# Kernel tuning notes

Hardware: AMD Instinct MI355X
Metric: run time of the kernel (lower is better)

## Reference

```python
import jax, jax.numpy as jnp
import numpy as np

EMBED = 2048
NUM_HEADS = 32
HEAD_DIM = EMBED // NUM_HEADS  # 64 (original head dim; sets the scaling)
RANK_KQ = 1024
RANK_V = 1024
DK = RANK_KQ // NUM_HEADS  # 32 low-rank kq head dim
DV = RANK_V // NUM_HEADS   # 32 low-rank v head dim
B, S = 2, 2048


def setup_inputs() -> dict:
    key = jax.random.key(0)
    ks = jax.random.split(key, 10)
    std = 0.02
    hidden_states = jax.random.normal(ks[0], (B, S, EMBED), dtype=jnp.float32)
    # causal additive mask, shape (B, 1, S, S) as asserted in forward
    neg = jnp.finfo(jnp.float32).min
    causal = jnp.where(jnp.tril(jnp.ones((S, S), dtype=bool)), 0.0, neg)
    attention_mask = jnp.broadcast_to(causal[None, None], (B, 1, S, S)).astype(jnp.float32)
    Wq = jax.random.normal(ks[1], (RANK_KQ, EMBED), dtype=jnp.float32) * std
    bq = jax.random.normal(ks[2], (RANK_KQ,), dtype=jnp.float32) * std
    Wk = jax.random.normal(ks[3], (RANK_KQ, EMBED), dtype=jnp.float32) * std
    bk = jax.random.normal(ks[4], (RANK_KQ,), dtype=jnp.float32) * std
    Wv = jax.random.normal(ks[5], (RANK_V, EMBED), dtype=jnp.float32) * std
    bv = jax.random.normal(ks[6], (RANK_V,), dtype=jnp.float32) * std
    Wo = jax.random.normal(ks[7], (EMBED, RANK_V), dtype=jnp.float32) * std
    bo = jax.random.normal(ks[8], (EMBED,), dtype=jnp.float32) * std
    return {"hidden_states": hidden_states, "attention_mask": attention_mask,
            "Wq": Wq, "bq": bq, "Wk": Wk, "bk": bk, "Wv": Wv, "bv": bv,
            "Wo": Wo, "bo": bo}


def reference(hidden_states, attention_mask, Wq, bq, Wk, bk, Wv, bv, Wo, bo):
    bsz, tgt_len, _ = hidden_states.shape
    scaling = HEAD_DIM ** (-0.5)  # uses ORIGINAL head_dim, not low-rank dim

    def split_heads(x, d):  # (b, s, H*d) -> (b, H, s, d)
        return x.reshape(bsz, -1, NUM_HEADS, d).transpose(0, 2, 1, 3)

    q = split_heads((hidden_states @ Wq.T + bq) * scaling, DK)
    k = split_heads(hidden_states @ Wk.T + bk, DK)
    v = split_heads(hidden_states @ Wv.T + bv, DV)

    # scores: (b, H, tgt, src)
    attn = jnp.einsum('bhqd,bhkd->bhqk', q, k)
    attn = attn + attention_mask  # broadcast over heads
    attn = jnp.maximum(attn, jnp.finfo(attn.dtype).min)
    attn = jax.nn.softmax(attn, axis=-1)

    out = jnp.einsum('bhqk,bhkd->bhqd', attn, v)  # (b, H, tgt, DV)
    out = out.transpose(0, 2, 1, 3).reshape(bsz, tgt_len, RANK_V)
    return out @ Wo.T + bo
```

## Files before the change

### kernel.cpp

```cpp
#include <hip/hip_runtime.h>
#include <stdint.h>

typedef __attribute__((ext_vector_type(8))) short bf16x8;
typedef __attribute__((ext_vector_type(4))) float f32x4;
typedef unsigned short ushort_t;

#define AS1 __attribute__((address_space(1)))
#define AS3 __attribute__((address_space(3)))

static __device__ __forceinline__ ushort_t f2b(float f) {
    union { float f; unsigned u; } x; x.f = f;
    unsigned r = x.u + 0x7fffu + ((x.u >> 16) & 1u);
    return (ushort_t)(r >> 16);
}
static __device__ __forceinline__ f32x4 mfma16(bf16x8 a, bf16x8 b, f32x4 c) {
    return __builtin_amdgcn_mfma_f32_16x16x32_bf16(a, b, c, 0, 0, 0);
}
static __device__ __forceinline__ void gl_lds16(const ushort_t* g, ushort_t* l) {
    __builtin_amdgcn_global_load_lds((const AS1 void*)g, (AS3 void*)l, 16, 0, 0);
}
static __device__ __forceinline__ unsigned pk2(float a, float b) {
    unsigned r;
    asm("v_cvt_pk_bf16_f32 %0, %1, %2" : "=v"(r) : "v"(a), "v"(b));
    return r;
}

__global__ __launch_bounds__(256)
void cvt_bf16(const float* __restrict__ s, ushort_t* __restrict__ d, int n8)
{
    int i = blockIdx.x * 256 + threadIdx.x;
    if (i >= n8) return;
    const float* p = s + (size_t)i * 8;
    f32x4 a = *(const f32x4*)p;
    f32x4 b = *(const f32x4*)(p + 4);
    bf16x8 r;
#pragma unroll
    for (int j = 0; j < 4; ++j) { r[j] = (short)f2b(a[j]); r[j+4] = (short)f2b(b[j]); }
    *(bf16x8*)(d + (size_t)i * 8) = r;
}

__global__ __launch_bounds__(256)
void cvt_w3(const float* __restrict__ wq, const float* __restrict__ wk,
            const float* __restrict__ wv, ushort_t* __restrict__ d)
{
    const float* s = (blockIdx.y == 0) ? wq : (blockIdx.y == 1) ? wk : wv;
    ushort_t* dst = d + (size_t)blockIdx.y * 2097152;
    int i = blockIdx.x * 256 + threadIdx.x;
    const float* p = s + (size_t)i * 8;
    f32x4 a = *(const f32x4*)p;
    f32x4 b = *(const f32x4*)(p + 4);
    bf16x8 r;
#pragma unroll
    for (int j = 0; j < 4; ++j) { r[j] = (short)f2b(a[j]); r[j+4] = (short)f2b(b[j]); }
    *(bf16x8*)(dst + (size_t)i * 8) = r;
}

__global__ __launch_bounds__(256, 2)
void gemm_nt(const ushort_t* __restrict__ A, const ushort_t* __restrict__ B,
             const float* __restrict__ b0, const float* __restrict__ b1,
             const float* __restrict__ b2, void* __restrict__ Cv,
             int M, int N, int K, float scale, int epi)
{
    __shared__ __align__(16) ushort_t As[128 * 32];
    __shared__ __align__(16) ushort_t Bs[128 * 32];
    const int tid = threadIdx.x;
    const int wave = tid >> 6, lane = tid & 63;
    const int l16 = lane & 15, quad = lane >> 4;
    const int bm = blockIdx.x * 128, bn = blockIdx.y * 128;
    const int wm = (wave >> 1) * 64, wn = (wave & 1) * 64;

    f32x4 acc[4][4];
#pragma unroll
    for (int i = 0; i < 4; ++i)
#pragma unroll
        for (int j = 0; j < 4; ++j) acc[i][j] = (f32x4){0.f, 0.f, 0.f, 0.f};

    for (int k0 = 0; k0 < K; k0 += 32) {
        __syncthreads();
#pragma unroll
        for (int i = 0; i < 2; ++i) {
            int chunk = i * 256 + tid;
            int row = chunk >> 2, c8 = chunk & 3;
            gl_lds16(A + (size_t)(bm + row) * K + k0 + c8 * 8, As + chunk * 8);
            gl_lds16(B + (size_t)(bn + row) * K + k0 + c8 * 8, Bs + chunk * 8);
        }
        __syncthreads();
        bf16x8 af[4], bfr[4];
#pragma unroll
        for (int i = 0; i < 4; ++i)
            af[i] = *(const bf16x8*)(As + (wm + i * 16 + l16) * 32 + quad * 8);
#pragma unroll
        for (int j = 0; j < 4; ++j)
            bfr[j] = *(const bf16x8*)(Bs + (wn + j * 16 + l16) * 32 + quad * 8);
#pragma unroll
        for (int i = 0; i < 4; ++i)
#pragma unroll
            for (int j = 0; j < 4; ++j)
                acc[i][j] = mfma16(af[i], bfr[j], acc[i][j]);
    }

#pragma unroll
    for (int i = 0; i < 4; ++i) {
#pragma unroll
        for (int j = 0; j < 4; ++j) {
            int col = bn + wn + j * 16 + l16;
            if (epi == 0) {
                float bvs = b0[col];
#pragma unroll
                for (int r = 0; r < 4; ++r) {
                    int row = bm + wm + i * 16 + quad * 4 + r;
                    ((float*)Cv)[(size_t)row * N + col] = (acc[i][j][r] + bvs) * scale;
                }
            } else {
                int mat = col >> 10, nc = col & 1023;
                const float* bp = (mat == 0) ? b0 : (mat == 1) ? b1 : b2;
                float bvs = bp[nc];
                int h = nc >> 5, d = nc & 31;
                if (mat == 2) {
                    int row0 = bm + wm + i * 16 + quad * 4;
                    int b = row0 >> 11, s = row0 & 2047;
                    ushort_t* dst = (ushort_t*)Cv + (size_t)2 * 4194304
                                  + ((size_t)(b * 32 + h) * 32 + d) * 2048 + s;
                    uint2 w;
                    w.x = ((unsigned)f2b(acc[i][j][1] + bvs) << 16) | f2b(acc[i][j][0] + bvs);
                    w.y = ((unsigned)f2b(acc[i][j][3] + bvs) << 16) | f2b(acc[i][j][2] + bvs);
                    *(uint2*)dst = w;
                } else {
                    float sc = (mat == 0) ? 0.125f : 1.0f;
                    ushort_t* dst = (ushort_t*)Cv + (size_t)mat * 4194304;
#pragma unroll
                    for (int r = 0; r < 4; ++r) {
                        int row = bm + wm + i * 16 + quad * 4 + r;
                        int b = row >> 11, s = row & 2047;
                        float v = (acc[i][j][r] + bvs) * sc;
                        dst[(((size_t)(b * 32 + h) * 2048 + s) << 5) + d] = f2b(v);
                    }
                }
            }
        }
    }
}

__global__ __launch_bounds__(512, 1)
void gemm8b(const ushort_t* __restrict__ A, const ushort_t* __restrict__ B,
            const float* __restrict__ bias, float* __restrict__ C,
            int M, int N, int K, float scale)
{
    __shared__ __align__(16) ushort_t lds[49152];
    const int tid = threadIdx.x;
    const int wave = tid >> 6, lane = tid & 63;
    const int l16 = lane & 15, quad = lane >> 4;
    const int wr = wave >> 2, wc = wave & 3;
    const int bm = blockIdx.x * 128, bn = blockIdx.y * 256;
    const int xo = (l16 & 8) << 1;
    const int S = K >> 4;
    const int NT = K >> 7;

    f32x4 acc[4][4];
#pragma unroll
    for (int i = 0; i < 4; ++i)
#pragma unroll
        for (int j = 0; j < 4; ++j) acc[i][j] = (f32x4){0.f,0.f,0.f,0.f};

    auto stg = [&](int s_) {
        int r = s_ & 7;
        ushort_t* ldst = lds + (r >> 1) * 12288 + (r & 1) * 8192;
        int ko = (s_ >> 1) << 5;
        if (s_ & 1) {
            int c = tid;
            int cl = c ^ (((c >> 5) & 1) << 1);
            gl_lds16(A + (size_t)(bm + (cl >> 2)) * K + ko + (cl & 3) * 8,
                     ldst + c * 8);
        } else {
#pragma unroll
            for (int call = 0; call < 2; ++call) {
                int c = call * 512 + tid;
                int cl = c ^ (((c >> 5) & 1) << 1);
                gl_lds16(B + (size_t)(bn + (cl >> 2)) * K + ko + (cl & 3) * 8,
                         ldst + c * 8);
            }
        }
    };

#pragma unroll
    for (int s0 = 0; s0 < 7; ++s0) stg(s0);
    asm volatile("s_waitcnt vmcnt(5)" ::: "memory");
    __builtin_amdgcn_s_barrier();

    for (int t = 0; t < NT; ++t) {
        const bool lastit = (t == NT - 1);
        bf16x8 bfr[4], af[2];
#pragma unroll
        for (int p = 0; p < 8; ++p) {
            asm volatile("" ::: "memory");
            const int offB = (p >> 1) * 12288;
            const int offA = offB + 8192;
            if ((p & 1) == 0) {
#pragma unroll
                for (int j = 0; j < 4; ++j)
                    bfr[j] = *(const bf16x8*)(lds + offB
                              + (wc * 64 + j * 16 + l16) * 32 + ((quad * 8) ^ xo));
            }
#pragma unroll
            for (int m = 0; m < 2; ++m)
                af[m] = *(const bf16x8*)(lds + offA
                          + (wr * 64 + (p & 1) * 32 + m * 16 + l16) * 32
                          + ((quad * 8) ^ xo));
            { int s_ = 8 * t + 7 + p; if (s_ < S) stg(s_); }
            __builtin_amdgcn_s_barrier();
            asm volatile("s_waitcnt lgkmcnt(0)" ::: "memory");
            __builtin_amdgcn_sched_barrier(0);
            __builtin_amdgcn_s_setprio(1);
#pragma unroll
            for (int m = 0; m < 2; ++m)
#pragma unroll
                for (int j = 0; j < 4; ++j)
                    acc[(p & 1) * 2 + m][j] =
                        mfma16(af[m], bfr[j], acc[(p & 1) * 2 + m][j]);
            __builtin_amdgcn_s_setprio(0);
            if (p == 3) {
                if (lastit) asm volatile("s_waitcnt vmcnt(0)" ::: "memory");
                else        asm volatile("s_waitcnt vmcnt(5)" ::: "memory");
            } else if (p == 7) {
                if (!lastit) asm volatile("s_waitcnt vmcnt(5)" ::: "memory");
            }
            __builtin_amdgcn_s_barrier();
        }
    }

#pragma unroll
    for (int i = 0; i < 4; ++i) {
#pragma unroll
        for (int j = 0; j < 4; ++j) {
            int col = bn + wc * 64 + j * 16 + l16;
            float bvs = bias[col];
#pragma unroll
            for (int r = 0; r < 4; ++r) {
                int row = bm + wr * 64 + i * 16 + quad * 4 + r;
                C[(size_t)row * N + col] = (acc[i][j][r] + bvs) * scale;
            }
        }
    }
}

__global__ __launch_bounds__(256, 4)
void attn(const ushort_t* __restrict__ Q, const ushort_t* __restrict__ Kg,
          const ushort_t* __restrict__ VT, ushort_t* __restrict__ Ctx)
{
    __shared__ __align__(16) ushort_t Ps[4][32 * 72];
    const int tid = threadIdx.x, wave = tid >> 6, lane = tid & 63;
    const int l16 = lane & 15, quad = lane >> 4, quad4 = quad * 4;
    const int bh = blockIdx.x;
    const int pr = blockIdx.y;
    const ushort_t* Qh = Q  + (size_t)bh * 2048 * 32;
    const ushort_t* Kh = Kg + (size_t)bh * 2048 * 32;
    const ushort_t* Vh = VT + (size_t)bh * 32 * 2048;
    const int b = bh >> 5, h = bh & 31;
    ushort_t* P0 = &Ps[wave][0];

    for (int half = 0; half < 2; ++half) {
        const int qt = half ? (15 - pr) : pr;
        const int q0 = qt * 128 + wave * 32;

        bf16x8 qf0 = *(const bf16x8*)(Qh + (size_t)(q0 + l16) * 32 + quad * 8);
        bf16x8 qf1 = *(const bf16x8*)(Qh + (size_t)(q0 + 16 + l16) * 32 + quad * 8);

        f32x4 o00 = (f32x4){0.f,0.f,0.f,0.f}, o01 = o00, o10 = o00, o11 = o00;
        float rs0 = 0.f, rs1 = 0.f;

        const int nchw = ((q0 + 31) >> 6) + 1;
        for (int c = 0; c < nchw; ++c) {
            const int kv0 = c * 64;
            bf16x8 kf[4];
#pragma unroll
            for (int t = 0; t < 4; ++t)
                kf[t] = *(const bf16x8*)(Kh + (size_t)(kv0 + t * 16 + l16) * 32 + quad * 8);
            f32x4 st0[4], st1[4];
#pragma unroll
            for (int t = 0; t < 4; ++t) {
                st0[t] = mfma16(kf[t], qf0, (f32x4){0.f,0.f,0.f,0.f});
                st1[t] = mfma16(kf[t], qf1, (f32x4){0.f,0.f,0.f,0.f});
            }
            bf16x8 vA0 = *(const bf16x8*)(Vh + (size_t)l16 * 2048 + kv0 + quad * 8);
            bf16x8 vA1 = *(const bf16x8*)(Vh + (size_t)l16 * 2048 + kv0 + 32 + quad * 8);
            bf16x8 vB0 = *(const bf16x8*)(Vh + (size_t)(16 + l16) * 2048 + kv0 + quad * 8);
            bf16x8 vB1 = *(const bf16x8*)(Vh + (size_t)(16 + l16) * 2048 + kv0 + 32 + quad * 8);

            const int qk0 = q0 + l16 - kv0;
            auto softmax_pack = [&](bool masked) {
#pragma unroll
                for (int t = 0; t < 4; ++t) {
                    float p0[4], p1[4];
#pragma unroll
                    for (int r = 0; r < 4; ++r) {
                        const int kk = t * 16 + quad4 + r;
                        float e0 = __expf(st0[t][r]);
                        float e1 = __expf(st1[t][r]);
                        p0[r] = (!masked || kk <= qk0)      ? e0 : 0.f;
                        p1[r] = (!masked || kk <= qk0 + 16) ? e1 : 0.f;
                        rs0 += p0[r]; rs1 += p1[r];
                    }
                    uint2 w0, w1;
                    w0.x = pk2(p0[0], p0[1]); w0.y = pk2(p0[2], p0[3]);
                    w1.x = pk2(p1[0], p1[1]); w1.y = pk2(p1[2], p1[3]);
                    *(uint2*)(P0 + (size_t)l16 * 72 + t * 16 + quad4) = w0;
                    *(uint2*)(P0 + (size_t)(16 + l16) * 72 + t * 16 + quad4) = w1;
                }
            };
            if (kv0 + 63 <= q0) softmax_pack(false); else softmax_pack(true);

            asm volatile("s_waitcnt lgkmcnt(0)" ::: "memory");
#pragma unroll
            for (int ks = 0; ks < 2; ++ks) {
                bf16x8 pa0 = *(const bf16x8*)(P0 + (size_t)l16 * 72 + ks * 32 + quad * 8);
                bf16x8 pa1 = *(const bf16x8*)(P0 + (size_t)(16 + l16) * 72 + ks * 32 + quad * 8);
                bf16x8 va = ks ? vA1 : vA0;
                bf16x8 vb = ks ? vB1 : vB0;
                o00 = mfma16(pa0, va, o00);
                o01 = mfma16(pa0, vb, o01);
                o10 = mfma16(pa1, va, o10);
                o11 = mfma16(pa1, vb, o11);
            }
        }

        rs0 += __shfl_xor(rs0, 16); rs0 += __shfl_xor(rs0, 32);
        rs1 += __shfl_xor(rs1, 16); rs1 += __shfl_xor(rs1, 32);

#pragma unroll
        for (int r = 0; r < 4; ++r) {
            const int qr = q0 + quad4 + r;
            float inv0 = 1.0f / __shfl(rs0, quad4 + r);
            float inv1 = 1.0f / __shfl(rs1, quad4 + r);
            size_t base0 = ((size_t)b * 2048 + qr) * 1024 + h * 32;
            size_t base1 = ((size_t)b * 2048 + qr + 16) * 1024 + h * 32;
            Ctx[base0 + l16]      = f2b(o00[r] * inv0);
            Ctx[base0 + 16 + l16] = f2b(o01[r] * inv0);
            Ctx[base1 + l16]      = f2b(o10[r] * inv1);
            Ctx[base1 + 16 + l16] = f2b(o11[r] * inv1);
        }
    }
}

extern "C" void kernel_launch(void* const* d_in, const int* in_sizes, int n_in,
                              void* d_out, int out_size, void* d_ws, size_t ws_size,
                              hipStream_t stream)
{
    const float* H  = (const float*)d_in[0];
    const float* Wq = (const float*)d_in[2];
    const float* bq = (const float*)d_in[3];
    const float* Wk = (const float*)d_in[4];
    const float* bk = (const float*)d_in[5];
    const float* Wv = (const float*)d_in[6];
    const float* bv = (const float*)d_in[7];
    const float* Wo = (const float*)d_in[8];
    const float* bo = (const float*)d_in[9];

    ushort_t* Hb   = (ushort_t*)d_ws;
    ushort_t* Wcat = Hb   + (size_t)8388608;
    ushort_t* Qb   = Wcat + (size_t)6291456;
    ushort_t* Kb   = Qb   + (size_t)4194304;
    ushort_t* Vtb  = Kb   + (size_t)4194304;
    ushort_t* Ctx  = Vtb  + (size_t)4194304;
    ushort_t* Wob  = Hb;

    dim3 blk(256, 1, 1);
    hipLaunchKernelGGL(cvt_bf16, dim3(4096, 1, 1), blk, 0, stream, H, Hb, 1048576);
    hipLaunchKernelGGL(cvt_w3, dim3(1024, 3, 1), blk, 0, stream, Wq, Wk, Wv, Wcat);

    hipLaunchKernelGGL(gemm_nt, dim3(32, 24, 1), blk, 0, stream,
                       Hb, Wcat, bq, bk, bv, (void*)Qb, 4096, 3072, 2048, 1.0f, 2);

    hipLaunchKernelGGL(cvt_bf16, dim3(1024, 1, 1), blk, 0, stream, Wo, Wob, 262144);

    hipLaunchKernelGGL(attn, dim3(64, 8, 1), blk, 0, stream, Qb, Kb, Vtb, Ctx);

    hipLaunchKernelGGL(gemm8b, dim3(32, 8, 1), dim3(512, 1, 1), 0, stream,
                       Ctx, Wob, bo, (float*)d_out, 4096, 2048, 1024, 1.0f);
}
```

Measured before the change: 279.8 us.

## Triple-buffer QKV GEMM LDS loads with swizzle and single barrier per step

Rewrites the QKV projection GEMM to use a three-slot LDS ring, prefetching tiles two k-steps ahead with global_load_lds and waiting on vmcnt, so only one barrier per iteration is needed. It XOR-swizzles the LDS layout to reduce bank conflicts on fragment reads, raises the MFMA priority during compute, and raises the launch-bounds occupancy hint to 3 blocks. The goal is to hide global-load latency behind the MFMAs, at the cost of more LDS per block and hand-tuned waitcnt logic that must stay correct.

```diff
diff --git a/kernel.cpp b/kernel.cpp
--- a/kernel.cpp
+++ b/kernel.cpp
@@ -55,19 +55,20 @@
     *(bf16x8*)(dst + (size_t)i * 8) = r;
 }
 
-__global__ __launch_bounds__(256, 2)
-void gemm_nt(const ushort_t* __restrict__ A, const ushort_t* __restrict__ B,
+__global__ __launch_bounds__(256, 3)
+void gemm_p2(const ushort_t* __restrict__ A, const ushort_t* __restrict__ B,
              const float* __restrict__ b0, const float* __restrict__ b1,
              const float* __restrict__ b2, void* __restrict__ Cv,
              int M, int N, int K, float scale, int epi)
 {
-    __shared__ __align__(16) ushort_t As[128 * 32];
-    __shared__ __align__(16) ushort_t Bs[128 * 32];
+    __shared__ __align__(16) ushort_t lds[24576];
     const int tid = threadIdx.x;
     const int wave = tid >> 6, lane = tid & 63;
     const int l16 = lane & 15, quad = lane >> 4;
     const int bm = blockIdx.x * 128, bn = blockIdx.y * 128;
     const int wm = (wave >> 1) * 64, wn = (wave & 1) * 64;
+    const int xo = (l16 & 8) << 1;
+    const int NT = K >> 5;
 
     f32x4 acc[4][4];
 #pragma unroll
@@ -75,28 +76,51 @@
 #pragma unroll
         for (int j = 0; j < 4; ++j) acc[i][j] = (f32x4){0.f, 0.f, 0.f, 0.f};
 
-    for (int k0 = 0; k0 < K; k0 += 32) {
-        __syncthreads();
-#pragma unroll
-        for (int i = 0; i < 2; ++i) {
-            int chunk = i * 256 + tid;
-            int row = chunk >> 2, c8 = chunk & 3;
-            gl_lds16(A + (size_t)(bm + row) * K + k0 + c8 * 8, As + chunk * 8);
-            gl_lds16(B + (size_t)(bn + row) * K + k0 + c8 * 8, Bs + chunk * 8);
-        }
-        __syncthreads();
+    auto stg = [&](int sl, int rp) {
+        int ko = sl << 5;
+#pragma unroll
+        for (int call = 0; call < 2; ++call) {
+            int c = call * 256 + tid;
+            int cl = c ^ (((c >> 5) & 1) << 1);
+            int row = cl >> 2, c8 = cl & 3;
+            gl_lds16(A + (size_t)(bm + row) * K + ko + c8 * 8,
+                     lds + rp * 8192 + c * 8);
+            gl_lds16(B + (size_t)(bn + row) * K + ko + c8 * 8,
+                     lds + rp * 8192 + 4096 + c * 8);
+        }
+    };
+
+    stg(0, 0);
+    stg(1, 1);
+    asm volatile("s_waitcnt vmcnt(4)" ::: "memory");
+    __builtin_amdgcn_s_barrier();
+
+    int ra = 0, rs = 2;
+    for (int s = 0; s < NT; ++s) {
+        if (s + 2 < NT) stg(s + 2, rs);
         bf16x8 af[4], bfr[4];
 #pragma unroll
         for (int i = 0; i < 4; ++i)
-            af[i] = *(const bf16x8*)(As + (wm + i * 16 + l16) * 32 + quad * 8);
+            af[i] = *(const bf16x8*)(lds + ra * 8192
+                      + (wm + i * 16 + l16) * 32 + ((quad * 8) ^ xo));
 #pragma unroll
         for (int j = 0; j < 4; ++j)
-            bfr[j] = *(const bf16x8*)(Bs + (wn + j * 16 + l16) * 32 + quad * 8);
+            bfr[j] = *(const bf16x8*)(lds + ra * 8192 + 4096
+                      + (wn + j * 16 + l16) * 32 + ((quad * 8) ^ xo));
+        asm volatile("s_waitcnt lgkmcnt(0)" ::: "memory");
+        __builtin_amdgcn_sched_barrier(0);
+        __builtin_amdgcn_s_setprio(1);
 #pragma unroll
         for (int i = 0; i < 4; ++i)
 #pragma unroll
             for (int j = 0; j < 4; ++j)
                 acc[i][j] = mfma16(af[i], bfr[j], acc[i][j]);
+        __builtin_amdgcn_s_setprio(0);
+        if (s == NT - 2) asm volatile("s_waitcnt vmcnt(0)" ::: "memory");
+        else             asm volatile("s_waitcnt vmcnt(4)" ::: "memory");
+        __builtin_amdgcn_s_barrier();
+        ra = (ra == 2) ? 0 : ra + 1;
+        rs = (rs == 2) ? 0 : rs + 1;
     }
 
 #pragma unroll
@@ -118,9 +142,9 @@
                 int h = nc >> 5, d = nc & 31;
                 if (mat == 2) {
                     int row0 = bm + wm + i * 16 + quad * 4;
-                    int b = row0 >> 11, s = row0 & 2047;
+                    int b = row0 >> 11, s2 = row0 & 2047;
                     ushort_t* dst = (ushort_t*)Cv + (size_t)2 * 4194304
-                                  + ((size_t)(b * 32 + h) * 32 + d) * 2048 + s;
+                                  + ((size_t)(b * 32 + h) * 32 + d) * 2048 + s2;
                     uint2 w;
                     w.x = ((unsigned)f2b(acc[i][j][1] + bvs) << 16) | f2b(acc[i][j][0] + bvs);
                     w.y = ((unsigned)f2b(acc[i][j][3] + bvs) << 16) | f2b(acc[i][j][2] + bvs);
@@ -131,9 +155,9 @@
 #pragma unroll
                     for (int r = 0; r < 4; ++r) {
                         int row = bm + wm + i * 16 + quad * 4 + r;
-                        int b = row >> 11, s = row & 2047;
+                        int b = row >> 11, s2 = row & 2047;
                         float v = (acc[i][j][r] + bvs) * sc;
-                        dst[(((size_t)(b * 32 + h) * 2048 + s) << 5) + d] = f2b(v);
+                        dst[(((size_t)(b * 32 + h) * 2048 + s2) << 5) + d] = f2b(v);
                     }
                 }
             }
@@ -367,7 +391,7 @@
     hipLaunchKernelGGL(cvt_bf16, dim3(4096, 1, 1), blk, 0, stream, H, Hb, 1048576);
     hipLaunchKernelGGL(cvt_w3, dim3(1024, 3, 1), blk, 0, stream, Wq, Wk, Wv, Wcat);
 
-    hipLaunchKernelGGL(gemm_nt, dim3(32, 24, 1), blk, 0, stream,
+    hipLaunchKernelGGL(gemm_p2, dim3(32, 24, 1), blk, 0, stream,
                        Hb, Wcat, bq, bk, bv, (void*)Qb, 4096, 3072, 2048, 1.0f, 2);
 
     hipLaunchKernelGGL(cvt_bf16, dim3(1024, 1, 1), blk, 0, stream, Wo, Wob, 262144);
```

New measurement: 282.5 us. No clear change (+1.0%).
